# Performance work log

Measured on AMD Instinct MI355X. Metric: run time of the kernel, lower is better.

Reference implementation:

```python
import jax, jax.numpy as jnp
import numpy as np


def setup_inputs() -> dict:
    key = jax.random.key(0)
    kq, kk, kv = jax.random.split(key, 3)
    B, Nq, Nk, d = 16, 4096, 4096, 128
    return {
        "query": jax.random.normal(kq, (B, Nq, d), dtype=jnp.float32),
        "key": jax.random.normal(kk, (B, Nk, d), dtype=jnp.float32),
        "value": jax.random.normal(kv, (B, Nk, d), dtype=jnp.float32),
    }


def reference(query, key, value):
    # weights = softmax(QK^T / sqrt(d)) with causal mask; dropout p=0.0 is identity
    d = key.shape[-1]
    scale = 1.0 / jnp.sqrt(jnp.asarray(d, dtype=query.dtype))
    scores = jnp.einsum("bqd,bkd->bqk", query, key) * scale  # [B, Nq, Nk]
    Nq, Nk = scores.shape[-2], scores.shape[-1]
    causal = jnp.tril(jnp.ones((Nq, Nk), dtype=bool))
    scores = jnp.where(causal, scores, jnp.asarray(-jnp.inf, dtype=scores.dtype))
    weights = jax.nn.softmax(scores, axis=-1)
    return jnp.einsum("bqk,bkv->bqv", weights, value)
```

## Files before the change

kernel.cpp:

```cpp
#include <hip/hip_runtime.h>
#include <stdint.h>


#define NB 16
#define NS 4096
#define DH 128
#define FRAG_U16 8192

typedef float          fx4   __attribute__((ext_vector_type(4)));
typedef uint32_t       ux4   __attribute__((ext_vector_type(4)));
typedef __bf16         bfv8  __attribute__((ext_vector_type(8)));
typedef __bf16         bfv4  __attribute__((ext_vector_type(4)));
typedef unsigned short u16x4 __attribute__((ext_vector_type(4)));

typedef const uint32_t __attribute__((address_space(1))) glob_u32;
typedef uint32_t       __attribute__((address_space(3))) lds_u32;

__device__ __forceinline__ fx4 mfma16(bfv8 a, bfv8 b, fx4 c) {
  return __builtin_amdgcn_mfma_f32_16x16x32_bf16(a, b, c, 0, 0, 0);
}

__global__ void __launch_bounds__(256) prepack_kernel(
    const float* __restrict__ K, const float* __restrict__ V,
    unsigned short* __restrict__ Kf, unsigned short* __restrict__ Vf) {
  __shared__ __align__(16) unsigned short tile[64][136];
  const int bid = blockIdx.x;
  const int b = bid >> 6, kvblk = bid & 63;
  const int kvb = kvblk << 6;
  const int tid = threadIdx.x;
  const size_t fbase = ((size_t)(b * 64 + kvblk)) * FRAG_U16;

  {
    const int tt = tid >> 6, lane = tid & 63;
    const int ln16 = lane & 15, g = lane >> 4;
    const float* kp = K + (((size_t)(b * NS + kvb + 16 * tt + ln16)) << 7) + 8 * g;
    unsigned short* op = Kf + fbase + tt * 2048 + lane * 8;
#pragma unroll
    for (int c = 0; c < 4; ++c) {
      fx4 a0 = *(const fx4*)(kp + 32 * c);
      fx4 a1 = *(const fx4*)(kp + 32 * c + 4);
      bfv8 t;
#pragma unroll
      for (int j = 0; j < 4; ++j) {
        t[j]     = (__bf16)a0[j];
        t[j + 4] = (__bf16)a1[j];
      }
      *(ux4*)(op + c * 512) = __builtin_bit_cast(ux4, t);
    }
  }

  {
    const int r = tid >> 2, cq = tid & 3;
    const float* vp = V + (((size_t)(b * NS + kvb + r)) << 7) + 32 * cq;
#pragma unroll
    for (int h = 0; h < 4; ++h) {
      fx4 f0 = *(const fx4*)(vp + 8 * h);
      fx4 f1 = *(const fx4*)(vp + 8 * h + 4);
      bfv8 t;
#pragma unroll
      for (int j = 0; j < 4; ++j) {
        t[j]     = (__bf16)f0[j];
        t[j + 4] = (__bf16)f1[j];
      }
      *(ux4*)&tile[r][32 * cq + 8 * h] = __builtin_bit_cast(ux4, t);
    }
  }
  __syncthreads();
  {
    const int dt = tid >> 5, c = (tid >> 4) & 1, ln16 = tid & 15;
    const int d = 16 * dt + ln16;
    unsigned short* op = Vf + fbase + dt * 1024 + c * 512 + ln16 * 8;
#pragma unroll
    for (int g = 0; g < 4; ++g) {
      unsigned short e[8];
#pragma unroll
      for (int j = 0; j < 4; ++j) {
        e[j]     = tile[32 * c + 4 * g + j][d];
        e[j + 4] = tile[32 * c + 16 + 4 * g + j][d];
      }
      *(ux4*)(op + g * 128) = *(const ux4*)e;
    }
  }
}

__global__ void __launch_bounds__(256, 3) attn_kernel(
    const float* __restrict__ Q, const unsigned short* __restrict__ Kf,
    const unsigned short* __restrict__ Vf, float* __restrict__ O,
    unsigned short* __restrict__ Pa, float* __restrict__ Ml, int split) {
  __shared__ __align__(16) unsigned char sm[32768];

  const int wid  = blockIdx.x;
  const int tid  = threadIdx.x;
  const int w    = tid >> 6;
  const int lane = tid & 63;
  const int g    = lane >> 4;
  const int ln16 = lane & 15;

  int b, t, j0, nc, mode;
  if (split) {
    const int slot = wid >> 8;
    const int v    = (wid >> 4) & 15;
    b = wid & 15;
    if (slot == 0) {
      t = v; j0 = 0; nc = 2 * v + 2; mode = 0;
    } else {
      t = 31 - v;
      j0 = (slot == 1) ? 0 : (t + 1);
      nc = t + 1;
      mode = slot;
    }
  } else {
    const int half = wid >> 8, ii = wid & 255;
    b = ii & 15;
    const int qi = ii >> 4;
    t = half ? qi : 31 - qi;
    j0 = 0; nc = 2 * t + 2; mode = 0;
  }

  const float SCALE = 0.12753102f;
  const fx4 z4 = {0.f, 0.f, 0.f, 0.f};

  const unsigned short* kfb = Kf + ((size_t)b * 64) * FRAG_U16;
  const unsigned short* vfb = Vf + ((size_t)b * 64) * FRAG_U16;

  const int qb = t << 7;
  const int qw = qb + 32 * w;

  bfv8 qf[2][4];
#pragma unroll
  for (int qt = 0; qt < 2; ++qt) {
#pragma unroll
    for (int c = 0; c < 4; ++c) {
      const float* qp = Q + (((size_t)(b * NS + qw + qt * 16 + ln16)) << 7) + 32 * c + 8 * g;
      fx4 a0 = *(const fx4*)qp;
      fx4 a1 = *(const fx4*)(qp + 4);
      bfv8 tt_;
#pragma unroll
      for (int j = 0; j < 4; ++j) {
        tt_[j]     = (__bf16)(a0[j] * SCALE);
        tt_[j + 4] = (__bf16)(a1[j] * SCALE);
      }
      qf[qt][c] = tt_;
    }
  }

  fx4 acc[2][8];
#pragma unroll
  for (int qt = 0; qt < 2; ++qt)
#pragma unroll
    for (int dt = 0; dt < 8; ++dt) acc[qt][dt] = z4;
  float mrun[2] = {-1e30f, -1e30f};
  float lsum[2] = {0.f, 0.f};

  const int nkvw = ((qw + 31) >> 6) + 1;
  const int jend = j0 + nc;

#define STAGE(jb)                                                              \
  do {                                                                         \
    const unsigned char* gk = (const unsigned char*)(kfb + (size_t)(jb)*FRAG_U16); \
    const unsigned char* gv = (const unsigned char*)(vfb + (size_t)(jb)*FRAG_U16); \
    _Pragma("unroll")                                                          \
    for (int ii = 0; ii < 4; ++ii) {                                           \
      const int off = ii * 4096 + w * 1024;                                    \
      __builtin_amdgcn_global_load_lds((glob_u32*)(gk + off + lane * 16),      \
                                       (lds_u32*)(sm + off), 16, 0, 0);        \
      __builtin_amdgcn_global_load_lds((glob_u32*)(gv + off + lane * 16),      \
                                       (lds_u32*)(sm + 16384 + off), 16, 0, 0); \
    }                                                                          \
  } while (0)

  STAGE(j0);
  asm volatile("s_waitcnt vmcnt(0)" ::: "memory");
  __builtin_amdgcn_s_barrier();
  asm volatile("" ::: "memory");

  for (int jb = j0; jb < jend; ++jb) {
    if (jb < nkvw) {
      const unsigned char* kb = sm;
      const unsigned char* vb = sm + 16384;

      fx4 s[2][4];
#pragma unroll
      for (int tt = 0; tt < 4; ++tt) { s[0][tt] = z4; s[1][tt] = z4; }
      __builtin_amdgcn_s_setprio(1);
#pragma unroll
      for (int tt = 0; tt < 4; ++tt) {
#pragma unroll
        for (int c = 0; c < 4; ++c) {
          bfv8 kfr = *(const bfv8*)(kb + tt * 4096 + c * 1024 + lane * 16);
          s[0][tt] = mfma16(kfr, qf[0][c], s[0][tt]);
          s[1][tt] = mfma16(kfr, qf[1][c], s[1][tt]);
        }
      }
      __builtin_amdgcn_s_setprio(0);

      const int kvb = jb << 6;
      if (kvb + 63 > qw) {
#pragma unroll
        for (int qt = 0; qt < 2; ++qt) {
          const int qrow = qw + qt * 16 + ln16;
#pragma unroll
          for (int tt = 0; tt < 4; ++tt)
#pragma unroll
            for (int r = 0; r < 4; ++r) {
              int kvpos = kvb + 16 * tt + 4 * g + r;
              if (kvpos > qrow) s[qt][tt][r] = -1e30f;
            }
        }
      }

      bfv8 pb[2][2];
#pragma unroll
      for (int qt = 0; qt < 2; ++qt) {
        fx4 m4 = __builtin_elementwise_max(
            __builtin_elementwise_max(s[qt][0], s[qt][1]),
            __builtin_elementwise_max(s[qt][2], s[qt][3]));
        float pm = fmaxf(fmaxf(m4[0], m4[1]), fmaxf(m4[2], m4[3]));
        pm = fmaxf(pm, __shfl_xor(pm, 16));
        pm = fmaxf(pm, __shfl_xor(pm, 32));
        float mq = mrun[qt];
        if (__any(pm > mq + 8.0f)) {
          float mn = fmaxf(mq, pm);
          float f  = __builtin_amdgcn_exp2f(mq - mn);
          lsum[qt] *= f;
#pragma unroll
          for (int dt = 0; dt < 8; ++dt) acc[qt][dt] *= f;
          mrun[qt] = mn;
          mq = mn;
        }
#pragma unroll
        for (int tt = 0; tt < 4; ++tt)
#pragma unroll
          for (int r = 0; r < 4; ++r)
            s[qt][tt][r] = __builtin_amdgcn_exp2f(s[qt][tt][r] - mq);
        fx4 r4 = (s[qt][0] + s[qt][1]) + (s[qt][2] + s[qt][3]);
        float rs = (r4[0] + r4[1]) + (r4[2] + r4[3]);
        rs += __shfl_xor(rs, 16);
        rs += __shfl_xor(rs, 32);
        lsum[qt] += rs;
#pragma unroll
        for (int c = 0; c < 2; ++c) {
          bfv8 tt_;
#pragma unroll
          for (int j = 0; j < 4; ++j) {
            tt_[j]     = (__bf16)s[qt][2 * c][j];
            tt_[j + 4] = (__bf16)s[qt][2 * c + 1][j];
          }
          pb[qt][c] = tt_;
        }
      }

      __builtin_amdgcn_s_setprio(1);
#pragma unroll
      for (int dt = 0; dt < 8; ++dt) {
#pragma unroll
        for (int c = 0; c < 2; ++c) {
          bfv8 vfr = *(const bfv8*)(vb + dt * 2048 + c * 1024 + lane * 16);
          acc[0][dt] = mfma16(vfr, pb[0][c], acc[0][dt]);
          acc[1][dt] = mfma16(vfr, pb[1][c], acc[1][dt]);
        }
      }
      __builtin_amdgcn_s_setprio(0);
    }

    asm volatile("" ::: "memory");
    __builtin_amdgcn_s_barrier();
    if (jb + 1 < jend) {
      STAGE(jb + 1);
      asm volatile("s_waitcnt vmcnt(0)" ::: "memory");
    }
    __builtin_amdgcn_s_barrier();
    asm volatile("" ::: "memory");
  }
#undef STAGE

  if (mode == 0) {
#pragma unroll
    for (int qt = 0; qt < 2; ++qt) {
      float inv = 1.0f / lsum[qt];
      float* ob = O + (((size_t)(b * NS + qw + qt * 16 + ln16)) << 7) + 4 * g;
#pragma unroll
      for (int dt = 0; dt < 8; ++dt) *(fx4*)(ob + 16 * dt) = acc[qt][dt] * inv;
    }
  } else {
    if (mode == 1) {
#pragma unroll
      for (int qt = 0; qt < 2; ++qt) {
        float* ob = O + (((size_t)(b * NS + qw + qt * 16 + ln16)) << 7) + 4 * g;
#pragma unroll
        for (int dt = 0; dt < 8; ++dt) *(fx4*)(ob + 16 * dt) = acc[qt][dt];
      }
    } else {
#pragma unroll
      for (int qt = 0; qt < 2; ++qt) {
        const int row = 32 * w + 16 * qt + ln16;
        unsigned short* pp =
            Pa + (((size_t)((b * 16 + (t - 16)) * 128 + row)) << 7) + 4 * g;
#pragma unroll
        for (int dt = 0; dt < 8; ++dt) {
          bfv4 t4;
#pragma unroll
          for (int j = 0; j < 4; ++j) t4[j] = (__bf16)acc[qt][dt][j];
          *(u16x4*)(pp + 16 * dt) = __builtin_bit_cast(u16x4, t4);
        }
      }
    }
    if (g == 0) {
      const int slot = mode - 1;
      float* mlp = Ml + (size_t)(((b * 16 + (t - 16)) * 2 + slot) * 2) * 128;
#pragma unroll
      for (int qt = 0; qt < 2; ++qt) {
        const int row = 32 * w + 16 * qt + ln16;
        mlp[row]       = mrun[qt];
        mlp[128 + row] = lsum[qt];
      }
    }
  }
}

__global__ void __launch_bounds__(256) merge_kernel(
    float* __restrict__ O, const unsigned short* __restrict__ Pa,
    const float* __restrict__ Ml) {
  const int gid = blockIdx.x * 256 + threadIdx.x;
  const int d4  = gid & 31;
  const int rg  = gid >> 5;
  const int b   = rg >> 11;
  const int r2  = rg & 2047;
  const int tt  = r2 >> 7;
  const int row = r2 & 127;

  const float* mlp = Ml + (size_t)((b * 16 + tt) * 4) * 128;
  const float m1 = mlp[row],       l1 = mlp[128 + row];
  const float m2 = mlp[256 + row], l2 = mlp[384 + row];
  const float m  = fmaxf(m1, m2);
  const float w1 = __builtin_amdgcn_exp2f(m1 - m);
  const float w2 = __builtin_amdgcn_exp2f(m2 - m);

  float* op = O + (((size_t)(b * NS + (16 + tt) * 128 + row)) << 7) + 4 * d4;
  fx4 a1 = *(const fx4*)op;
  const unsigned short* pp =
      Pa + (((size_t)((b * 16 + tt) * 128 + row)) << 7) + 4 * d4;
  bfv4 a2b = __builtin_bit_cast(bfv4, *(const u16x4*)pp);
  fx4 a2;
#pragma unroll
  for (int j = 0; j < 4; ++j) a2[j] = (float)a2b[j];

  const float inv = 1.0f / (w1 * l1 + w2 * l2);
  fx4 o = (a1 * w1 + a2 * w2) * inv;
  *(fx4*)op = o;
}

extern "C" void kernel_launch(void* const* d_in, const int* in_sizes, int n_in,
                              void* d_out, int out_size, void* d_ws, size_t ws_size,
                              hipStream_t stream) {
  (void)in_sizes; (void)n_in; (void)out_size;
  const float* Q = (const float*)d_in[0];
  const float* K = (const float*)d_in[1];
  const float* V = (const float*)d_in[2];
  float* O = (float*)d_out;

  unsigned short* Kf = (unsigned short*)d_ws;
  unsigned short* Vf = Kf + (size_t)NB * NS * DH;
  unsigned short* Pa = Vf + (size_t)NB * NS * DH;
  float*          Ml = (float*)((char*)d_ws + 41943040);

  const size_t NEED = 41943040 + 524288;
  const int split = (ws_size >= NEED) ? 1 : 0;

  prepack_kernel<<<dim3(NB * 64), dim3(256), 0, stream>>>(K, V, Kf, Vf);
  attn_kernel<<<dim3(split ? 768 : 512), dim3(256), 0, stream>>>(
      Q, Kf, Vf, O, Pa, Ml, split);
  if (split) merge_kernel<<<dim3(4096), dim3(256), 0, stream>>>(O, Pa, Ml);
}
```

Before: 124.3 us.

## Double-buffer 32-key KV tiles and rebalance split-K work across 768 blocks

Halves the KV tile to 32 keys and double-buffers K/V in LDS, issuing the next tile's global-to-LDS load before computing the current one, which drops one barrier per iteration. Work is redistributed so each block handles a fixed 44-tile chunk of a combined long/short query-tile pair, with some blocks chaining into a second query tile. The merge kernel now combines up to three partials. This aims to even out the load across blocks and overlap memory with compute, at the cost of more iterations, extra partial writes and more complex indexing.

```diff
diff --git a/kernel.cpp b/kernel.cpp
--- a/kernel.cpp
+++ b/kernel.cpp
@@ -96,226 +96,237 @@
   const int g    = lane >> 4;
   const int ln16 = lane & 15;
 
-  int b, t, j0, nc, mode;
+  int b;
+  int t, u0, un, mode, pidx, slot;
+  int t1 = 0, u1a = 0, u1b = 0, m1v = 0;
+  int again = 0;
+
   if (split) {
-    const int slot = wid >> 8;
-    const int v    = (wid >> 4) & 15;
+    const int n = wid >> 4;
     b = wid & 15;
-    if (slot == 0) {
-      t = v; j0 = 0; nc = 2 * v + 2; mode = 0;
+    const int v = n / 3;
+    const int k = n - 3 * v;
+    const int L = 128 - 4 * v;
+    const int st = 44 * k, en = st + 44;
+    if (st < L) {
+      t = 31 - v; u0 = st; un = (en < L) ? en : L;
+      mode = (k == 0) ? 1 : 2;
+      slot = k;
+      pidx = (t <= 21) ? (t - 11) : (11 + 2 * (t - 22) + (k - 1));
+      if (en > L) {
+        t1 = v; u1a = 0; u1b = en - L;
+        m1v = (v <= 10) ? 0 : 1;
+        again = 1;
+      }
     } else {
-      t = 31 - v;
-      j0 = (slot == 1) ? 0 : (t + 1);
-      nc = t + 1;
-      mode = slot;
+      t = v; u0 = st - L; un = en - L;
+      const int s = (u0 > 0) ? 1 : 0;
+      mode = (v <= 10) ? 0 : ((s == 0) ? 1 : 2);
+      slot = s;
+      pidx = v - 11;
     }
   } else {
     const int half = wid >> 8, ii = wid & 255;
     b = ii & 15;
     const int qi = ii >> 4;
     t = half ? qi : 31 - qi;
-    j0 = 0; nc = 2 * t + 2; mode = 0;
+    u0 = 0; un = 4 * t + 4; mode = 0; pidx = 0; slot = 0;
   }
 
   const float SCALE = 0.12753102f;
   const fx4 z4 = {0.f, 0.f, 0.f, 0.f};
 
-  const unsigned short* kfb = Kf + ((size_t)b * 64) * FRAG_U16;
-  const unsigned short* vfb = Vf + ((size_t)b * 64) * FRAG_U16;
-
-  const int qb = t << 7;
-  const int qw = qb + 32 * w;
-
-  bfv8 qf[2][4];
-#pragma unroll
-  for (int qt = 0; qt < 2; ++qt) {
-#pragma unroll
-    for (int c = 0; c < 4; ++c) {
-      const float* qp = Q + (((size_t)(b * NS + qw + qt * 16 + ln16)) << 7) + 32 * c + 8 * g;
-      fx4 a0 = *(const fx4*)qp;
-      fx4 a1 = *(const fx4*)(qp + 4);
-      bfv8 tt_;
-#pragma unroll
-      for (int j = 0; j < 4; ++j) {
-        tt_[j]     = (__bf16)(a0[j] * SCALE);
-        tt_[j + 4] = (__bf16)(a1[j] * SCALE);
-      }
-      qf[qt][c] = tt_;
-    }
-  }
-
-  fx4 acc[2][8];
-#pragma unroll
-  for (int qt = 0; qt < 2; ++qt)
-#pragma unroll
-    for (int dt = 0; dt < 8; ++dt) acc[qt][dt] = z4;
-  float mrun[2] = {-1e30f, -1e30f};
-  float lsum[2] = {0.f, 0.f};
-
-  const int nkvw = ((qw + 31) >> 6) + 1;
-  const int jend = j0 + nc;
-
-#define STAGE(jb)                                                              \
+  const unsigned char* kfB = (const unsigned char*)Kf + (size_t)b * 1048576;
+  const unsigned char* vfB = (const unsigned char*)Vf + (size_t)b * 1048576;
+
+#define STAGE(jb, bo)                                                          \
   do {                                                                         \
-    const unsigned char* gk = (const unsigned char*)(kfb + (size_t)(jb)*FRAG_U16); \
-    const unsigned char* gv = (const unsigned char*)(vfb + (size_t)(jb)*FRAG_U16); \
+    const unsigned char* gk = kfB + (size_t)(jb) * 8192;                       \
+    const unsigned char* gv = vfB + (size_t)((jb) >> 1) * 16384 + ((jb) & 1) * 1024; \
     _Pragma("unroll")                                                          \
-    for (int ii = 0; ii < 4; ++ii) {                                           \
-      const int off = ii * 4096 + w * 1024;                                    \
-      __builtin_amdgcn_global_load_lds((glob_u32*)(gk + off + lane * 16),      \
-                                       (lds_u32*)(sm + off), 16, 0, 0);        \
-      __builtin_amdgcn_global_load_lds((glob_u32*)(gv + off + lane * 16),      \
-                                       (lds_u32*)(sm + 16384 + off), 16, 0, 0); \
+    for (int ii = 0; ii < 2; ++ii) {                                           \
+      __builtin_amdgcn_global_load_lds(                                        \
+          (glob_u32*)(gk + w * 2048 + ii * 1024 + lane * 16),                  \
+          (lds_u32*)(sm + (bo) + w * 2048 + ii * 1024), 16, 0, 0);             \
+      const int dt_ = 2 * w + ii;                                              \
+      __builtin_amdgcn_global_load_lds(                                        \
+          (glob_u32*)(gv + dt_ * 2048 + lane * 16),                            \
+          (lds_u32*)(sm + (bo) + 8192 + dt_ * 1024), 16, 0, 0);                \
     }                                                                          \
   } while (0)
 
-  STAGE(j0);
-  asm volatile("s_waitcnt vmcnt(0)" ::: "memory");
-  __builtin_amdgcn_s_barrier();
-  asm volatile("" ::: "memory");
-
-  for (int jb = j0; jb < jend; ++jb) {
-    if (jb < nkvw) {
-      const unsigned char* kb = sm;
-      const unsigned char* vb = sm + 16384;
-
-      fx4 s[2][4];
-#pragma unroll
-      for (int tt = 0; tt < 4; ++tt) { s[0][tt] = z4; s[1][tt] = z4; }
-      __builtin_amdgcn_s_setprio(1);
-#pragma unroll
-      for (int tt = 0; tt < 4; ++tt) {
-#pragma unroll
-        for (int c = 0; c < 4; ++c) {
-          bfv8 kfr = *(const bfv8*)(kb + tt * 4096 + c * 1024 + lane * 16);
-          s[0][tt] = mfma16(kfr, qf[0][c], s[0][tt]);
-          s[1][tt] = mfma16(kfr, qf[1][c], s[1][tt]);
-        }
-      }
-      __builtin_amdgcn_s_setprio(0);
-
-      const int kvb = jb << 6;
-      if (kvb + 63 > qw) {
-#pragma unroll
-        for (int qt = 0; qt < 2; ++qt) {
-          const int qrow = qw + qt * 16 + ln16;
-#pragma unroll
-          for (int tt = 0; tt < 4; ++tt)
-#pragma unroll
-            for (int r = 0; r < 4; ++r) {
-              int kvpos = kvb + 16 * tt + 4 * g + r;
-              if (kvpos > qrow) s[qt][tt][r] = -1e30f;
-            }
-        }
-      }
-
-      bfv8 pb[2][2];
-#pragma unroll
-      for (int qt = 0; qt < 2; ++qt) {
-        fx4 m4 = __builtin_elementwise_max(
-            __builtin_elementwise_max(s[qt][0], s[qt][1]),
-            __builtin_elementwise_max(s[qt][2], s[qt][3]));
-        float pm = fmaxf(fmaxf(m4[0], m4[1]), fmaxf(m4[2], m4[3]));
-        pm = fmaxf(pm, __shfl_xor(pm, 16));
-        pm = fmaxf(pm, __shfl_xor(pm, 32));
-        float mq = mrun[qt];
-        if (__any(pm > mq + 8.0f)) {
-          float mn = fmaxf(mq, pm);
-          float f  = __builtin_amdgcn_exp2f(mq - mn);
-          lsum[qt] *= f;
-#pragma unroll
-          for (int dt = 0; dt < 8; ++dt) acc[qt][dt] *= f;
-          mrun[qt] = mn;
-          mq = mn;
-        }
-#pragma unroll
-        for (int tt = 0; tt < 4; ++tt)
-#pragma unroll
-          for (int r = 0; r < 4; ++r)
-            s[qt][tt][r] = __builtin_amdgcn_exp2f(s[qt][tt][r] - mq);
-        fx4 r4 = (s[qt][0] + s[qt][1]) + (s[qt][2] + s[qt][3]);
-        float rs = (r4[0] + r4[1]) + (r4[2] + r4[3]);
-        rs += __shfl_xor(rs, 16);
-        rs += __shfl_xor(rs, 32);
-        lsum[qt] += rs;
-#pragma unroll
-        for (int c = 0; c < 2; ++c) {
-          bfv8 tt_;
-#pragma unroll
-          for (int j = 0; j < 4; ++j) {
-            tt_[j]     = (__bf16)s[qt][2 * c][j];
-            tt_[j + 4] = (__bf16)s[qt][2 * c + 1][j];
-          }
-          pb[qt][c] = tt_;
-        }
-      }
-
-      __builtin_amdgcn_s_setprio(1);
-#pragma unroll
-      for (int dt = 0; dt < 8; ++dt) {
-#pragma unroll
-        for (int c = 0; c < 2; ++c) {
-          bfv8 vfr = *(const bfv8*)(vb + dt * 2048 + c * 1024 + lane * 16);
-          acc[0][dt] = mfma16(vfr, pb[0][c], acc[0][dt]);
-          acc[1][dt] = mfma16(vfr, pb[1][c], acc[1][dt]);
-        }
-      }
-      __builtin_amdgcn_s_setprio(0);
-    }
-
-    asm volatile("" ::: "memory");
-    __builtin_amdgcn_s_barrier();
-    if (jb + 1 < jend) {
-      STAGE(jb + 1);
-      asm volatile("s_waitcnt vmcnt(0)" ::: "memory");
-    }
+  for (;;) {
+    const int qw = (t << 7) + 32 * w;
+
+    bfv8 qf[2][4];
+#pragma unroll
+    for (int qt = 0; qt < 2; ++qt) {
+#pragma unroll
+      for (int c = 0; c < 4; ++c) {
+        const float* qp = Q + (((size_t)(b * NS + qw + qt * 16 + ln16)) << 7) + 32 * c + 8 * g;
+        fx4 a0 = *(const fx4*)qp;
+        fx4 a1 = *(const fx4*)(qp + 4);
+        bfv8 tt_;
+#pragma unroll
+        for (int j = 0; j < 4; ++j) {
+          tt_[j]     = (__bf16)(a0[j] * SCALE);
+          tt_[j + 4] = (__bf16)(a1[j] * SCALE);
+        }
+        qf[qt][c] = tt_;
+      }
+    }
+
+    fx4 acc[2][8];
+#pragma unroll
+    for (int qt = 0; qt < 2; ++qt)
+#pragma unroll
+      for (int dt = 0; dt < 8; ++dt) acc[qt][dt] = z4;
+    float mrun[2] = {-1e30f, -1e30f};
+    float lsum[2] = {0.f, 0.f};
+
+    const int nkvw = (qw >> 5) + 1;
+
+    STAGE(u0, 0);
+    asm volatile("s_waitcnt vmcnt(0)" ::: "memory");
     __builtin_amdgcn_s_barrier();
     asm volatile("" ::: "memory");
+
+    int cur = 0;
+    for (int jb = u0; jb < un; ++jb) {
+      if (jb + 1 < un) STAGE(jb + 1, (cur ^ 1) * 16384);
+
+      if (jb < nkvw) {
+        const unsigned char* kb = sm + cur * 16384;
+        const unsigned char* vb = kb + 8192;
+
+        fx4 s[2][2];
+        s[0][0] = z4; s[0][1] = z4; s[1][0] = z4; s[1][1] = z4;
+        __builtin_amdgcn_s_setprio(1);
+#pragma unroll
+        for (int tt = 0; tt < 2; ++tt) {
+#pragma unroll
+          for (int c = 0; c < 4; ++c) {
+            bfv8 kfr = *(const bfv8*)(kb + tt * 4096 + c * 1024 + lane * 16);
+            s[0][tt] = mfma16(kfr, qf[0][c], s[0][tt]);
+            s[1][tt] = mfma16(kfr, qf[1][c], s[1][tt]);
+          }
+        }
+        __builtin_amdgcn_s_setprio(0);
+
+        const int kvb = jb << 5;
+        if (kvb + 31 > qw) {
+#pragma unroll
+          for (int qt = 0; qt < 2; ++qt) {
+            const int qrow = qw + qt * 16 + ln16;
+#pragma unroll
+            for (int tt = 0; tt < 2; ++tt)
+#pragma unroll
+              for (int r = 0; r < 4; ++r) {
+                int kvpos = kvb + 16 * tt + 4 * g + r;
+                if (kvpos > qrow) s[qt][tt][r] = -1e30f;
+              }
+          }
+        }
+
+        bfv8 pb[2];
+#pragma unroll
+        for (int qt = 0; qt < 2; ++qt) {
+          fx4 m4 = __builtin_elementwise_max(s[qt][0], s[qt][1]);
+          float pm = fmaxf(fmaxf(m4[0], m4[1]), fmaxf(m4[2], m4[3]));
+          pm = fmaxf(pm, __shfl_xor(pm, 16));
+          pm = fmaxf(pm, __shfl_xor(pm, 32));
+          float mq = mrun[qt];
+          if (__any(pm > mq + 8.0f)) {
+            float mn = fmaxf(mq, pm);
+            float f  = __builtin_amdgcn_exp2f(mq - mn);
+            lsum[qt] *= f;
+#pragma unroll
+            for (int dt = 0; dt < 8; ++dt) acc[qt][dt] *= f;
+            mrun[qt] = mn;
+            mq = mn;
+          }
+#pragma unroll
+          for (int tt = 0; tt < 2; ++tt)
+#pragma unroll
+            for (int r = 0; r < 4; ++r)
+              s[qt][tt][r] = __builtin_amdgcn_exp2f(s[qt][tt][r] - mq);
+          fx4 r4 = s[qt][0] + s[qt][1];
+          float rs = (r4[0] + r4[1]) + (r4[2] + r4[3]);
+          rs += __shfl_xor(rs, 16);
+          rs += __shfl_xor(rs, 32);
+          lsum[qt] += rs;
+          bfv8 tt_;
+#pragma unroll
+          for (int j = 0; j < 4; ++j) {
+            tt_[j]     = (__bf16)s[qt][0][j];
+            tt_[j + 4] = (__bf16)s[qt][1][j];
+          }
+          pb[qt] = tt_;
+        }
+
+        __builtin_amdgcn_s_setprio(1);
+#pragma unroll
+        for (int dt = 0; dt < 8; ++dt) {
+          bfv8 vfr = *(const bfv8*)(vb + dt * 1024 + lane * 16);
+          acc[0][dt] = mfma16(vfr, pb[0], acc[0][dt]);
+          acc[1][dt] = mfma16(vfr, pb[1], acc[1][dt]);
+        }
+        __builtin_amdgcn_s_setprio(0);
+      }
+
+      asm volatile("s_waitcnt vmcnt(0)" ::: "memory");
+      __builtin_amdgcn_s_barrier();
+      asm volatile("" ::: "memory");
+      cur ^= 1;
+    }
+
+    if (mode == 0) {
+#pragma unroll
+      for (int qt = 0; qt < 2; ++qt) {
+        float inv = 1.0f / lsum[qt];
+        float* ob = O + (((size_t)(b * NS + qw + qt * 16 + ln16)) << 7) + 4 * g;
+#pragma unroll
+        for (int dt = 0; dt < 8; ++dt) *(fx4*)(ob + 16 * dt) = acc[qt][dt] * inv;
+      }
+    } else {
+      if (mode == 1) {
+#pragma unroll
+        for (int qt = 0; qt < 2; ++qt) {
+          float* ob = O + (((size_t)(b * NS + qw + qt * 16 + ln16)) << 7) + 4 * g;
+#pragma unroll
+          for (int dt = 0; dt < 8; ++dt) *(fx4*)(ob + 16 * dt) = acc[qt][dt];
+        }
+      } else {
+#pragma unroll
+        for (int qt = 0; qt < 2; ++qt) {
+          const int row = 32 * w + 16 * qt + ln16;
+          unsigned short* pp =
+              Pa + (((size_t)((b * 32 + pidx) * 128 + row)) << 7) + 4 * g;
+#pragma unroll
+          for (int dt = 0; dt < 8; ++dt) {
+            bfv4 t4;
+#pragma unroll
+            for (int j = 0; j < 4; ++j) t4[j] = (__bf16)acc[qt][dt][j];
+            *(u16x4*)(pp + 16 * dt) = __builtin_bit_cast(u16x4, t4);
+          }
+        }
+      }
+      if (g == 0) {
+        float* mlp = Ml + (size_t)((b * 32 + t) * 4 + slot) * 256;
+#pragma unroll
+        for (int qt = 0; qt < 2; ++qt) {
+          const int row = 32 * w + 16 * qt + ln16;
+          mlp[row]       = mrun[qt];
+          mlp[128 + row] = lsum[qt];
+        }
+      }
+    }
+
+    if (!again) break;
+    again = 0;
+    t = t1; u0 = u1a; un = u1b; mode = m1v; pidx = 0; slot = 0;
   }
 #undef STAGE
-
-  if (mode == 0) {
-#pragma unroll
-    for (int qt = 0; qt < 2; ++qt) {
-      float inv = 1.0f / lsum[qt];
-      float* ob = O + (((size_t)(b * NS + qw + qt * 16 + ln16)) << 7) + 4 * g;
-#pragma unroll
-      for (int dt = 0; dt < 8; ++dt) *(fx4*)(ob + 16 * dt) = acc[qt][dt] * inv;
-    }
-  } else {
-    if (mode == 1) {
-#pragma unroll
-      for (int qt = 0; qt < 2; ++qt) {
-        float* ob = O + (((size_t)(b * NS + qw + qt * 16 + ln16)) << 7) + 4 * g;
-#pragma unroll
-        for (int dt = 0; dt < 8; ++dt) *(fx4*)(ob + 16 * dt) = acc[qt][dt];
-      }
-    } else {
-#pragma unroll
-      for (int qt = 0; qt < 2; ++qt) {
-        const int row = 32 * w + 16 * qt + ln16;
-        unsigned short* pp =
-            Pa + (((size_t)((b * 16 + (t - 16)) * 128 + row)) << 7) + 4 * g;
-#pragma unroll
-        for (int dt = 0; dt < 8; ++dt) {
-          bfv4 t4;
-#pragma unroll
-          for (int j = 0; j < 4; ++j) t4[j] = (__bf16)acc[qt][dt][j];
-          *(u16x4*)(pp + 16 * dt) = __builtin_bit_cast(u16x4, t4);
-        }
-      }
-    }
-    if (g == 0) {
-      const int slot = mode - 1;
-      float* mlp = Ml + (size_t)(((b * 16 + (t - 16)) * 2 + slot) * 2) * 128;
-#pragma unroll
-      for (int qt = 0; qt < 2; ++qt) {
-        const int row = 32 * w + 16 * qt + ln16;
-        mlp[row]       = mrun[qt];
-        mlp[128 + row] = lsum[qt];
-      }
-    }
-  }
 }
 
 __global__ void __launch_bounds__(256) merge_kernel(
@@ -324,30 +335,48 @@
   const int gid = blockIdx.x * 256 + threadIdx.x;
   const int d4  = gid & 31;
   const int rg  = gid >> 5;
-  const int b   = rg >> 11;
-  const int r2  = rg & 2047;
-  const int tt  = r2 >> 7;
+  const int b   = rg / 2688;
+  const int r2  = rg - b * 2688;
+  const int ti  = r2 >> 7;
   const int row = r2 & 127;
-
-  const float* mlp = Ml + (size_t)((b * 16 + tt) * 4) * 128;
-  const float m1 = mlp[row],       l1 = mlp[128 + row];
-  const float m2 = mlp[256 + row], l2 = mlp[384 + row];
-  const float m  = fmaxf(m1, m2);
+  const int t   = 11 + ti;
+
+  const float* mlb = Ml + (size_t)((b * 32 + t) * 4) * 256;
+  const float m0 = mlb[row],       l0 = mlb[128 + row];
+  const float m1 = mlb[256 + row], l1 = mlb[384 + row];
+  const int three = (t >= 22);
+  float m2 = -1e30f, l2 = 0.f;
+  if (three) { m2 = mlb[512 + row]; l2 = mlb[640 + row]; }
+
+  const float m  = fmaxf(fmaxf(m0, m1), m2);
+  const float w0 = __builtin_amdgcn_exp2f(m0 - m);
   const float w1 = __builtin_amdgcn_exp2f(m1 - m);
-  const float w2 = __builtin_amdgcn_exp2f(m2 - m);
-
-  float* op = O + (((size_t)(b * NS + (16 + tt) * 128 + row)) << 7) + 4 * d4;
-  fx4 a1 = *(const fx4*)op;
-  const unsigned short* pp =
-      Pa + (((size_t)((b * 16 + tt) * 128 + row)) << 7) + 4 * d4;
-  bfv4 a2b = __builtin_bit_cast(bfv4, *(const u16x4*)pp);
-  fx4 a2;
-#pragma unroll
-  for (int j = 0; j < 4; ++j) a2[j] = (float)a2b[j];
-
-  const float inv = 1.0f / (w1 * l1 + w2 * l2);
-  fx4 o = (a1 * w1 + a2 * w2) * inv;
-  *(fx4*)op = o;
+
+  float* op = O + (((size_t)(b * NS + (t << 7) + row)) << 7) + 4 * d4;
+  fx4 a0 = *(const fx4*)op;
+
+  const int p1 = (t <= 21) ? (t - 11) : (11 + 2 * (t - 22));
+  const unsigned short* pp1 =
+      Pa + (((size_t)((b * 32 + p1) * 128 + row)) << 7) + 4 * d4;
+  bfv4 a1b = __builtin_bit_cast(bfv4, *(const u16x4*)pp1);
+  fx4 a1;
+#pragma unroll
+  for (int j = 0; j < 4; ++j) a1[j] = (float)a1b[j];
+
+  fx4 num   = a0 * w0 + a1 * w1;
+  float den = w0 * l0 + w1 * l1;
+  if (three) {
+    const float w2 = __builtin_amdgcn_exp2f(m2 - m);
+    const unsigned short* pp2 =
+        Pa + (((size_t)((b * 32 + p1 + 1) * 128 + row)) << 7) + 4 * d4;
+    bfv4 a2b = __builtin_bit_cast(bfv4, *(const u16x4*)pp2);
+    fx4 a2;
+#pragma unroll
+    for (int j = 0; j < 4; ++j) a2[j] = (float)a2b[j];
+    num += a2 * w2;
+    den += w2 * l2;
+  }
+  *(fx4*)op = num * (1.0f / den);
 }
 
 extern "C" void kernel_launch(void* const* d_in, const int* in_sizes, int n_in,
@@ -361,14 +390,14 @@
 
   unsigned short* Kf = (unsigned short*)d_ws;
   unsigned short* Vf = Kf + (size_t)NB * NS * DH;
-  unsigned short* Pa = Vf + (size_t)NB * NS * DH;
-  float*          Ml = (float*)((char*)d_ws + 41943040);
-
-  const size_t NEED = 41943040 + 524288;
+  unsigned short* Pa = (unsigned short*)((char*)d_ws + 33554432);
+  float*          Ml = (float*)((char*)d_ws + 50331648);
+
+  const size_t NEED = 52428800;
   const int split = (ws_size >= NEED) ? 1 : 0;
 
   prepack_kernel<<<dim3(NB * 64), dim3(256), 0, stream>>>(K, V, Kf, Vf);
   attn_kernel<<<dim3(split ? 768 : 512), dim3(256), 0, stream>>>(
       Q, Kf, Vf, O, Pa, Ml, split);
-  if (split) merge_kernel<<<dim3(4096), dim3(256), 0, stream>>>(O, Pa, Ml);
+  if (split) merge_kernel<<<dim3(5376), dim3(256), 0, stream>>>(O, Pa, Ml);
 }
```

After: 125.1 us. No clear change (+0.6%).

## Restructure attention into 512-thread blocks with 32-wide KV tiles and double buffering

Applied to the files above, without the earlier changes.

Rewrites the attention kernel so each block runs 8 waves of 16 query rows each and steps through 32-key KV sub-tiles. The KV tile is double-buffered in LDS so the next tile's global-to-LDS load overlaps compute, which removes one barrier per step. Work is rebalanced into 512 blocks: one piece covers the first half of a long tile, and the other covers the rest plus a short tile in a second pass. The V prepack layout is changed to match. This trades fewer MFMAs per LDS fragment read, since each wave now has one query tile instead of two, for more waves and latency hiding. A leftover no-op conditional remains in the code.

```diff
diff --git a/kernel.cpp b/kernel.cpp
--- a/kernel.cpp
+++ b/kernel.cpp
@@ -5,7 +5,6 @@
 #define NB 16
 #define NS 4096
 #define DH 128
-#define FRAG_U16 8192
 
 typedef float          fx4   __attribute__((ext_vector_type(4)));
 typedef uint32_t       ux4   __attribute__((ext_vector_type(4)));
@@ -28,7 +27,7 @@
   const int b = bid >> 6, kvblk = bid & 63;
   const int kvb = kvblk << 6;
   const int tid = threadIdx.x;
-  const size_t fbase = ((size_t)(b * 64 + kvblk)) * FRAG_U16;
+  const size_t fbase = ((size_t)(b * 64 + kvblk)) * 8192;
 
   {
     const int tt = tid >> 6, lane = tid & 63;
@@ -69,7 +68,7 @@
   {
     const int dt = tid >> 5, c = (tid >> 4) & 1, ln16 = tid & 15;
     const int d = 16 * dt + ln16;
-    unsigned short* op = Vf + fbase + dt * 1024 + c * 512 + ln16 * 8;
+    unsigned short* op = Vf + fbase + c * 4096 + dt * 512 + ln16 * 8;
 #pragma unroll
     for (int g = 0; g < 4; ++g) {
       unsigned short e[8];
@@ -83,7 +82,7 @@
   }
 }
 
-__global__ void __launch_bounds__(256, 3) attn_kernel(
+__global__ void __launch_bounds__(512, 4) attn_kernel(
     const float* __restrict__ Q, const unsigned short* __restrict__ Kf,
     const unsigned short* __restrict__ Vf, float* __restrict__ O,
     unsigned short* __restrict__ Pa, float* __restrict__ Ml, int split) {
@@ -96,42 +95,52 @@
   const int g    = lane >> 4;
   const int ln16 = lane & 15;
 
-  int b, t, j0, nc, mode;
+  int b, t, u0, un, mode;
+  int t1 = 0, u1b = 0;
+  int again = 0;
+
   if (split) {
-    const int slot = wid >> 8;
-    const int v    = (wid >> 4) & 15;
+    const int piece = wid >> 8;
+    const int v     = (wid >> 4) & 15;
     b = wid & 15;
-    if (slot == 0) {
-      t = v; j0 = 0; nc = 2 * v + 2; mode = 0;
+    t = 31 - v;
+    if (piece == 0) {
+      u0 = 0; un = 66; mode = 1;
     } else {
-      t = 31 - v;
-      j0 = (slot == 1) ? 0 : (t + 1);
-      nc = t + 1;
-      mode = slot;
+      u0 = 66; un = 128 - 4 * v; mode = 2;
+      t1 = v; u1b = 4 * v + 4; again = 1;
     }
   } else {
     const int half = wid >> 8, ii = wid & 255;
     b = ii & 15;
     const int qi = ii >> 4;
     t = half ? qi : 31 - qi;
-    j0 = 0; nc = 2 * t + 2; mode = 0;
+    u0 = 0; un = 4 * t + 4; mode = 0;
   }
 
   const float SCALE = 0.12753102f;
   const fx4 z4 = {0.f, 0.f, 0.f, 0.f};
 
-  const unsigned short* kfb = Kf + ((size_t)b * 64) * FRAG_U16;
-  const unsigned short* vfb = Vf + ((size_t)b * 64) * FRAG_U16;
-
-  const int qb = t << 7;
-  const int qw = qb + 32 * w;
-
-  bfv8 qf[2][4];
-#pragma unroll
-  for (int qt = 0; qt < 2; ++qt) {
+  const unsigned char* kfB = (const unsigned char*)Kf + (size_t)b * 1048576;
+  const unsigned char* vfB = (const unsigned char*)Vf + (size_t)b * 1048576;
+
+#define STAGE(jb, bo)                                                         \
+  do {                                                                        \
+    const unsigned char* gk = kfB + (size_t)(jb) * 8192;                      \
+    const unsigned char* gv = vfB + (size_t)(jb) * 8192;                      \
+    __builtin_amdgcn_global_load_lds((glob_u32*)(gk + w * 1024 + lane * 16),  \
+                                     (lds_u32*)(sm + (bo) + w * 1024), 16, 0, 0); \
+    __builtin_amdgcn_global_load_lds((glob_u32*)(gv + w * 1024 + lane * 16),  \
+                                     (lds_u32*)(sm + (bo) + 8192 + w * 1024), 16, 0, 0); \
+  } while (0)
+
+  for (;;) {
+    const int qw = (t << 7) + 16 * w;
+
+    bfv8 qf[4];
 #pragma unroll
     for (int c = 0; c < 4; ++c) {
-      const float* qp = Q + (((size_t)(b * NS + qw + qt * 16 + ln16)) << 7) + 32 * c + 8 * g;
+      const float* qp = Q + (((size_t)(b * NS + qw + ln16)) << 7) + 32 * c + 8 * g;
       fx4 a0 = *(const fx4*)qp;
       fx4 a1 = *(const fx4*)(qp + 4);
       bfv8 tt_;
@@ -140,182 +149,136 @@
         tt_[j]     = (__bf16)(a0[j] * SCALE);
         tt_[j + 4] = (__bf16)(a1[j] * SCALE);
       }
-      qf[qt][c] = tt_;
-    }
-  }
-
-  fx4 acc[2][8];
-#pragma unroll
-  for (int qt = 0; qt < 2; ++qt)
-#pragma unroll
-    for (int dt = 0; dt < 8; ++dt) acc[qt][dt] = z4;
-  float mrun[2] = {-1e30f, -1e30f};
-  float lsum[2] = {0.f, 0.f};
-
-  const int nkvw = ((qw + 31) >> 6) + 1;
-  const int jend = j0 + nc;
-
-#define STAGE(jb)                                                              \
-  do {                                                                         \
-    const unsigned char* gk = (const unsigned char*)(kfb + (size_t)(jb)*FRAG_U16); \
-    const unsigned char* gv = (const unsigned char*)(vfb + (size_t)(jb)*FRAG_U16); \
-    _Pragma("unroll")                                                          \
-    for (int ii = 0; ii < 4; ++ii) {                                           \
-      const int off = ii * 4096 + w * 1024;                                    \
-      __builtin_amdgcn_global_load_lds((glob_u32*)(gk + off + lane * 16),      \
-                                       (lds_u32*)(sm + off), 16, 0, 0);        \
-      __builtin_amdgcn_global_load_lds((glob_u32*)(gv + off + lane * 16),      \
-                                       (lds_u32*)(sm + 16384 + off), 16, 0, 0); \
-    }                                                                          \
-  } while (0)
-
-  STAGE(j0);
-  asm volatile("s_waitcnt vmcnt(0)" ::: "memory");
-  __builtin_amdgcn_s_barrier();
-  asm volatile("" ::: "memory");
-
-  for (int jb = j0; jb < jend; ++jb) {
-    if (jb < nkvw) {
-      const unsigned char* kb = sm;
-      const unsigned char* vb = sm + 16384;
-
-      fx4 s[2][4];
-#pragma unroll
-      for (int tt = 0; tt < 4; ++tt) { s[0][tt] = z4; s[1][tt] = z4; }
-      __builtin_amdgcn_s_setprio(1);
-#pragma unroll
-      for (int tt = 0; tt < 4; ++tt) {
-#pragma unroll
-        for (int c = 0; c < 4; ++c) {
-          bfv8 kfr = *(const bfv8*)(kb + tt * 4096 + c * 1024 + lane * 16);
-          s[0][tt] = mfma16(kfr, qf[0][c], s[0][tt]);
-          s[1][tt] = mfma16(kfr, qf[1][c], s[1][tt]);
-        }
-      }
-      __builtin_amdgcn_s_setprio(0);
-
-      const int kvb = jb << 6;
-      if (kvb + 63 > qw) {
-#pragma unroll
-        for (int qt = 0; qt < 2; ++qt) {
-          const int qrow = qw + qt * 16 + ln16;
-#pragma unroll
-          for (int tt = 0; tt < 4; ++tt)
+      qf[c] = tt_;
+    }
+
+    fx4 acc[8];
+#pragma unroll
+    for (int dt = 0; dt < 8; ++dt) acc[dt] = z4;
+    float mrun = -1e30f;
+    float lsum = 0.f;
+
+    const int nkvw = (qw >> 5) + 1;
+    const int qrow = qw + ln16;
+
+    STAGE(u0, 0);
+    asm volatile("s_waitcnt vmcnt(0)" ::: "memory");
+    __builtin_amdgcn_s_barrier();
+    asm volatile("" ::: "memory");
+
+    int cur = 0;
+    for (int jb = u0; jb < un; ++jb) {
+      if (jb + 1 < un) STAGE(jb + 1, (cur ^ 1) * 16384);
+
+      if (jb < nkvw) {
+        const unsigned char* kb = sm + cur * 16384;
+        const unsigned char* vb = kb + 8192;
+
+        fx4 s[2];
+        s[0] = z4; s[1] = z4;
+        __builtin_amdgcn_s_setprio(1);
+#pragma unroll
+        for (int tt = 0; tt < 2; ++tt) {
+#pragma unroll
+          for (int c = 0; c < 4; ++c) {
+            bfv8 kfr = *(const bfv8*)(kb + tt * 4096 + c * 1024 + lane * 16);
+            s[tt] = mfma16(kfr, qf[c], s[tt]);
+          }
+        }
+        __builtin_amdgcn_s_setprio(0);
+
+        const int kvb = jb << 5;
+        if (kvb + 31 > qrow - ln16 + 0 + (qw - qw) + qw - qw + qw % 1 + 31 * 0 + (qw & 0) ? (kvb + 31 > qw) : 0) {  }
+        if (kvb + 31 > qw) {
+#pragma unroll
+          for (int tt = 0; tt < 2; ++tt)
 #pragma unroll
             for (int r = 0; r < 4; ++r) {
               int kvpos = kvb + 16 * tt + 4 * g + r;
-              if (kvpos > qrow) s[qt][tt][r] = -1e30f;
+              if (kvpos > qrow) s[tt][r] = -1e30f;
             }
         }
-      }
-
-      bfv8 pb[2][2];
-#pragma unroll
-      for (int qt = 0; qt < 2; ++qt) {
-        fx4 m4 = __builtin_elementwise_max(
-            __builtin_elementwise_max(s[qt][0], s[qt][1]),
-            __builtin_elementwise_max(s[qt][2], s[qt][3]));
+
+        fx4 m4 = __builtin_elementwise_max(s[0], s[1]);
         float pm = fmaxf(fmaxf(m4[0], m4[1]), fmaxf(m4[2], m4[3]));
         pm = fmaxf(pm, __shfl_xor(pm, 16));
         pm = fmaxf(pm, __shfl_xor(pm, 32));
-        float mq = mrun[qt];
-        if (__any(pm > mq + 8.0f)) {
-          float mn = fmaxf(mq, pm);
-          float f  = __builtin_amdgcn_exp2f(mq - mn);
-          lsum[qt] *= f;
-#pragma unroll
-          for (int dt = 0; dt < 8; ++dt) acc[qt][dt] *= f;
-          mrun[qt] = mn;
-          mq = mn;
-        }
-#pragma unroll
-        for (int tt = 0; tt < 4; ++tt)
+        if (__any(pm > mrun + 8.0f)) {
+          float mn = fmaxf(mrun, pm);
+          float f  = __builtin_amdgcn_exp2f(mrun - mn);
+          lsum *= f;
+#pragma unroll
+          for (int dt = 0; dt < 8; ++dt) acc[dt] *= f;
+          mrun = mn;
+        }
+#pragma unroll
+        for (int tt = 0; tt < 2; ++tt)
 #pragma unroll
           for (int r = 0; r < 4; ++r)
-            s[qt][tt][r] = __builtin_amdgcn_exp2f(s[qt][tt][r] - mq);
-        fx4 r4 = (s[qt][0] + s[qt][1]) + (s[qt][2] + s[qt][3]);
+            s[tt][r] = __builtin_amdgcn_exp2f(s[tt][r] - mrun);
+        fx4 r4 = s[0] + s[1];
         float rs = (r4[0] + r4[1]) + (r4[2] + r4[3]);
         rs += __shfl_xor(rs, 16);
         rs += __shfl_xor(rs, 32);
-        lsum[qt] += rs;
-#pragma unroll
-        for (int c = 0; c < 2; ++c) {
-          bfv8 tt_;
-#pragma unroll
-          for (int j = 0; j < 4; ++j) {
-            tt_[j]     = (__bf16)s[qt][2 * c][j];
-            tt_[j + 4] = (__bf16)s[qt][2 * c + 1][j];
-          }
-          pb[qt][c] = tt_;
-        }
-      }
-
-      __builtin_amdgcn_s_setprio(1);
-#pragma unroll
-      for (int dt = 0; dt < 8; ++dt) {
-#pragma unroll
-        for (int c = 0; c < 2; ++c) {
-          bfv8 vfr = *(const bfv8*)(vb + dt * 2048 + c * 1024 + lane * 16);
-          acc[0][dt] = mfma16(vfr, pb[0][c], acc[0][dt]);
-          acc[1][dt] = mfma16(vfr, pb[1][c], acc[1][dt]);
-        }
-      }
-      __builtin_amdgcn_s_setprio(0);
-    }
-
-    asm volatile("" ::: "memory");
-    __builtin_amdgcn_s_barrier();
-    if (jb + 1 < jend) {
-      STAGE(jb + 1);
+        lsum += rs;
+        bfv8 pb;
+#pragma unroll
+        for (int j = 0; j < 4; ++j) {
+          pb[j]     = (__bf16)s[0][j];
+          pb[j + 4] = (__bf16)s[1][j];
+        }
+
+        __builtin_amdgcn_s_setprio(1);
+#pragma unroll
+        for (int dt = 0; dt < 8; ++dt) {
+          bfv8 vfr = *(const bfv8*)(vb + dt * 1024 + lane * 16);
+          acc[dt] = mfma16(vfr, pb, acc[dt]);
+        }
+        __builtin_amdgcn_s_setprio(0);
+      }
+
       asm volatile("s_waitcnt vmcnt(0)" ::: "memory");
-    }
-    __builtin_amdgcn_s_barrier();
-    asm volatile("" ::: "memory");
-  }
-#undef STAGE
-
-  if (mode == 0) {
-#pragma unroll
-    for (int qt = 0; qt < 2; ++qt) {
-      float inv = 1.0f / lsum[qt];
-      float* ob = O + (((size_t)(b * NS + qw + qt * 16 + ln16)) << 7) + 4 * g;
-#pragma unroll
-      for (int dt = 0; dt < 8; ++dt) *(fx4*)(ob + 16 * dt) = acc[qt][dt] * inv;
-    }
-  } else {
-    if (mode == 1) {
-#pragma unroll
-      for (int qt = 0; qt < 2; ++qt) {
-        float* ob = O + (((size_t)(b * NS + qw + qt * 16 + ln16)) << 7) + 4 * g;
-#pragma unroll
-        for (int dt = 0; dt < 8; ++dt) *(fx4*)(ob + 16 * dt) = acc[qt][dt];
-      }
+      __builtin_amdgcn_s_barrier();
+      asm volatile("" ::: "memory");
+      cur ^= 1;
+    }
+
+    if (mode == 0) {
+      float inv = 1.0f / lsum;
+      float* ob = O + (((size_t)(b * NS + qrow)) << 7) + 4 * g;
+#pragma unroll
+      for (int dt = 0; dt < 8; ++dt) *(fx4*)(ob + 16 * dt) = acc[dt] * inv;
     } else {
-#pragma unroll
-      for (int qt = 0; qt < 2; ++qt) {
-        const int row = 32 * w + 16 * qt + ln16;
+      if (mode == 1) {
+        float* ob = O + (((size_t)(b * NS + qrow)) << 7) + 4 * g;
+#pragma unroll
+        for (int dt = 0; dt < 8; ++dt) *(fx4*)(ob + 16 * dt) = acc[dt];
+      } else {
+        const int row = 16 * w + ln16;
         unsigned short* pp =
             Pa + (((size_t)((b * 16 + (t - 16)) * 128 + row)) << 7) + 4 * g;
 #pragma unroll
         for (int dt = 0; dt < 8; ++dt) {
           bfv4 t4;
 #pragma unroll
-          for (int j = 0; j < 4; ++j) t4[j] = (__bf16)acc[qt][dt][j];
+          for (int j = 0; j < 4; ++j) t4[j] = (__bf16)acc[dt][j];
           *(u16x4*)(pp + 16 * dt) = __builtin_bit_cast(u16x4, t4);
         }
       }
-    }
-    if (g == 0) {
-      const int slot = mode - 1;
-      float* mlp = Ml + (size_t)(((b * 16 + (t - 16)) * 2 + slot) * 2) * 128;
-#pragma unroll
-      for (int qt = 0; qt < 2; ++qt) {
-        const int row = 32 * w + 16 * qt + ln16;
-        mlp[row]       = mrun[qt];
-        mlp[128 + row] = lsum[qt];
-      }
-    }
-  }
+      if (g == 0) {
+        const int slot = mode - 1;
+        const int row = 16 * w + ln16;
+        float* mlp = Ml + (size_t)(((b * 16 + (t - 16)) * 2 + slot) * 2) * 128;
+        mlp[row]       = mrun;
+        mlp[128 + row] = lsum;
+      }
+    }
+
+    if (!again) break;
+    again = 0;
+    t = t1; u0 = 0; un = u1b; mode = 0;
+  }
+#undef STAGE
 }
 
 __global__ void __launch_bounds__(256) merge_kernel(
@@ -361,14 +324,13 @@
 
   unsigned short* Kf = (unsigned short*)d_ws;
   unsigned short* Vf = Kf + (size_t)NB * NS * DH;
-  unsigned short* Pa = Vf + (size_t)NB * NS * DH;
+  unsigned short* Pa = (unsigned short*)((char*)d_ws + 33554432);
   float*          Ml = (float*)((char*)d_ws + 41943040);
 
   const size_t NEED = 41943040 + 524288;
   const int split = (ws_size >= NEED) ? 1 : 0;
 
   prepack_kernel<<<dim3(NB * 64), dim3(256), 0, stream>>>(K, V, Kf, Vf);
-  attn_kernel<<<dim3(split ? 768 : 512), dim3(256), 0, stream>>>(
-      Q, Kf, Vf, O, Pa, Ml, split);
+  attn_kernel<<<dim3(512), dim3(512), 0, stream>>>(Q, Kf, Vf, O, Pa, Ml, split);
   if (split) merge_kernel<<<dim3(4096), dim3(256), 0, stream>>>(O, Pa, Ml);
 }
```

Result: no change. 124.5 us (+0.2%).
